# Performance work log

Hardware: AMD Instinct MI355X
Metric: run time of the kernel (lower is better)

The kernel has to match this reference:

```python
import jax, jax.numpy as jnp
import numpy as np

N, N_H = 256, 64          # detections per image, humans (permuted to top)
NUM_ITER = 2
E = 1024                   # node_encoding_size == box_feature_size
T_LIS, K_LIS, W_LIS = 8.3, 12.0, 10.0


def lis(x):
    # Low-grade Instance Suppression
    return T_LIS / (1.0 + jnp.exp(K_LIS - W_LIS * x))


def setup_inputs() -> dict:
    key = jax.random.key(0)
    ks = jax.random.split(key, 25)
    s = 0.02  # weight scale keeps sigmoid/relu in a sane range
    rn = lambda k, shape, sc=1.0: jax.random.normal(k, shape, jnp.float32) * sc
    inp = {}
    inp['box_features'] = rn(ks[0], (N, 12544))            # [N, 256*7*7]
    inp['node_spatial'] = rn(ks[1], (N, 1024))             # conv spatial-head output
    inp['scores'] = jax.random.uniform(ks[2], (N,), jnp.float32)
    labels = jax.random.randint(ks[3], (N,), 1, 80)
    inp['labels'] = labels.at[:N_H].set(0)                 # humans (idx 0) on top
    inp['class_mask'] = jax.random.bernoulli(ks[4], 0.2, (80, 117))
    inp['W_bh1'] = rn(ks[5], (12544, 1024), s); inp['b_bh1'] = jnp.zeros((1024,), jnp.float32)
    inp['W_bh2'] = rn(ks[6], (1024, 1024), s);  inp['b_bh2'] = jnp.zeros((1024,), jnp.float32)
    inp['W_sa']  = rn(ks[7], (1024, 1024), s)
    inp['W_a1']  = rn(ks[8], (4096, 2048), s); inp['b_a1'] = jnp.zeros((2048,), jnp.float32)
    inp['W_a2']  = rn(ks[9], (2048, 1024), s); inp['b_a2'] = jnp.zeros((1024,), jnp.float32)
    inp['W_a3']  = rn(ks[10], (1024, 1), s);   inp['b_a3'] = jnp.zeros((1,), jnp.float32)
    inp['W_hm']  = rn(ks[11], (1024, 1024), s); inp['b_hm'] = jnp.zeros((1024,), jnp.float32)
    inp['W_om']  = rn(ks[12], (1024, 1024), s); inp['b_om'] = jnp.zeros((1024,), jnp.float32)
    inp['W_hu']  = rn(ks[13], (2048, 1024), s)
    inp['W_ou']  = rn(ks[14], (2048, 1024), s)
    return inp


def _keep_indices():
    xv, yv = np.meshgrid(np.arange(N_H), np.arange(N), indexing='ij')
    m = (xv != yv).ravel()
    return jnp.asarray(xv.ravel()[m]), jnp.asarray(yv.ravel()[m])


def reference(box_features, node_spatial, scores, W_bh1, b_bh1, W_bh2, b_bh2,
              W_sa, W_a1, b_a1, W_a2, b_a2, W_a3, b_a3,
              W_hm, b_hm, W_om, b_om, W_hu, W_ou, labels, class_mask):
    # box_head: Flatten -> Linear -> ReLU -> Linear -> ReLU
    enc = jax.nn.relu(box_features @ W_bh1 + b_bh1)
    enc = jax.nn.relu(enc @ W_bh2 + b_bh2)                 # [N, E]
    h_enc = enc[:N_H]                                      # [N_H, E]
    h_sp = node_spatial[:N_H]                              # [N_H, 1024]
    # spatial_attention on pairwise spatial differences (fixed across iters)
    diff = node_spatial[None, :, :] - h_sp[:, None, :]     # [N_H, N, 1024]
    h_to_o = jnp.einsum('hnd,de->hne', diff, W_sa)         # Linear, no bias
    o_to_h = -h_to_o
    adj = jnp.ones((N_H, N), enc.dtype)
    for _ in range(NUM_ITER):
        # adjacency MLP + sigmoid over all n_h*n pairs
        hf = jnp.concatenate([h_enc, h_sp], axis=1)        # [N_H, 2048]
        of = jnp.concatenate([enc, node_spatial], axis=1)  # [N, 2048]
        pair_in = jnp.concatenate([
            jnp.broadcast_to(hf[:, None, :], (N_H, N, 2 * E)),
            jnp.broadcast_to(of[None, :, :], (N_H, N, 2 * E))], axis=-1)  # [N_H,N,4096]
        hdn = jax.nn.relu(pair_in @ W_a1 + b_a1)
        hdn = jax.nn.relu(hdn @ W_a2 + b_a2)
        adj = jax.nn.sigmoid((hdn @ W_a3 + b_a3)[..., 0])  # [N_H, N]
        # object -> human messages
        obj_msg = jax.nn.relu(enc @ W_om + b_om)           # [N, R]
        agg_o = (adj[..., None] * (obj_msg[None, :, :] * o_to_h)).sum(1)  # [N_H, R]
        h_enc = jnp.concatenate([h_enc, agg_o], axis=1) @ W_hu            # [N_H, E]
        # human -> object messages
        hum_msg = jax.nn.relu(h_enc @ W_hm + b_hm)         # [N_H, R]
        agg_h = (adj[..., None] * (hum_msg[:, None, :] * h_to_o)).sum(0)  # [N, R]
        enc = jnp.concatenate([enc, agg_h], axis=1) @ W_ou                # [N, E]
    x_keep, y_keep = _keep_indices()                       # [P], P = N_H*N - N_H
    pair_feats = jnp.concatenate([h_enc[x_keep], h_sp[x_keep],
                                  enc[y_keep], node_spatial[y_keep]], axis=1)  # [P, 4096]
    # prior scores: LIS(score_h)*LIS(score_o) scattered to valid target classes
    prod = lis(scores[x_keep]) * lis(scores[y_keep])       # [P]
    prior = prod[:, None] * class_mask[labels[y_keep]].astype(pair_feats.dtype)  # [P, 117]
    prior = adj[x_keep, y_keep][:, None] * prior
    return jnp.concatenate([pair_feats, prior], axis=1)    # [P, 4096+117]
```

## Files before the change

kernel.cpp:

```cpp
#include <hip/hip_runtime.h>

using bf16 = __bf16;
typedef __bf16 bf16x4 __attribute__((ext_vector_type(4)));
typedef __bf16 bf16x8 __attribute__((ext_vector_type(8)));
typedef float  f32x4  __attribute__((ext_vector_type(4)));

#define LDS_STRIDE 40
#define GST 40

__device__ __forceinline__ float ldf(const void* p, size_t i, int f32) {
    return f32 ? ((const float*)p)[i] : (float)((const bf16*)p)[i];
}
__device__ __forceinline__ bf16x8 ld8(const void* p, size_t i, int f32) {
    bf16x8 r;
    if (f32) {
        f32x4 a = *(const f32x4*)((const float*)p + i);
        f32x4 b = *(const f32x4*)((const float*)p + i + 4);
#pragma unroll
        for (int j = 0; j < 4; ++j) { r[j] = (bf16)a[j]; r[j + 4] = (bf16)b[j]; }
    } else {
        r = *(const bf16x8*)((const bf16*)p + i);
    }
    return r;
}
__device__ __forceinline__ void st1(void* p, size_t i, float v, int f32) {
    if (f32) ((float*)p)[i] = v;
    else     ((bf16*)p)[i] = (bf16)v;
}

__global__ void init_flag(int* __restrict__ dflag) { *dflag = 0; }

__global__ void detect_kernel(const unsigned short* __restrict__ p, int n,
                              int* __restrict__ dflag)
{
    const unsigned int* q = (const unsigned int*)p;
    const int nw = n >> 1;
    int hit = 0;
    for (int i = blockIdx.x * 256 + threadIdx.x; i < nw; i += gridDim.x * 256) {
        unsigned int w = q[i];
        if ((w & 0x7F80u) == 0x7F80u || (w & 0x7F800000u) == 0x7F800000u) hit = 1;
    }
    if (__any(hit) && (threadIdx.x & 63) == 0) atomicOr(dflag, 1);
}

__global__ void cvt_kernel(const void* __restrict__ src, bf16* __restrict__ dst,
                           int n, const int* __restrict__ dflag)
{
    const int f32 = *dflag;
    const int stride = gridDim.x * 256;
    if ((n & 7) == 0) {
        const int nv = n >> 3;
        for (int i = blockIdx.x * 256 + threadIdx.x; i < nv; i += stride) {
            bf16x8 v = ld8(src, (size_t)i * 8, f32);
            *(bf16x8*)(dst + (size_t)i * 8) = v;
        }
    } else {
        for (int i = blockIdx.x * 256 + threadIdx.x; i < n; i += stride)
            dst[i] = (bf16)ldf(src, i, f32);
    }
}

__global__ void transpose_any(const void* __restrict__ W, bf16* __restrict__ Wt,
                              int K, int N, const int* __restrict__ dflag)
{
    __shared__ bf16 tile[32][33];
    const int f32 = *dflag;
    const int n0 = blockIdx.x * 32, k0 = blockIdx.y * 32;
    const int tx = threadIdx.x, ty = threadIdx.y;
#pragma unroll
    for (int i = 0; i < 4; ++i)
        tile[ty + i * 8][tx] = (bf16)ldf(W, (size_t)(k0 + ty + i * 8) * N + n0 + tx, f32);
    __syncthreads();
#pragma unroll
    for (int i = 0; i < 4; ++i)
        Wt[(size_t)(n0 + ty + i * 8) * K + k0 + tx] = tile[tx][ty + i * 8];
}

__global__ __launch_bounds__(256)
void gemm_p(const bf16* __restrict__ A, int lda,
            const void* __restrict__ B, size_t boff, int ldb,
            float* __restrict__ part, int N, int Kc,
            const int* __restrict__ dflag)
{
    __shared__ bf16 As[64 * GST];
    __shared__ bf16 Bs[64 * GST];
    const int f32 = *dflag;
    const int t = threadIdx.x;
    const int l = t & 63;
    const int quad = l >> 4, lr = l & 15;
    const int w = t >> 6, wm = w >> 1, wn = w & 1;
    const int mBlock = blockIdx.y * 64, nBlock = blockIdx.x * 64;
    const int ar = t >> 2, ac = (t & 3) * 8;
    const int kr = t >> 3, nc = (t & 7) * 8;
    const int kBeg = blockIdx.z * Kc;
    const int nIter = Kc >> 5;

    f32x4 acc[2][2] = {};

    bf16x8 avr = *(const bf16x8*)(A + (size_t)(mBlock + ar) * lda + kBeg + ac);
    bf16x8 bvr = ld8(B, boff + (size_t)(kBeg + kr) * ldb + nBlock + nc, f32);

    for (int it = 0; it < nIter; ++it) {
        *(bf16x8*)&As[ar * GST + ac] = avr;
#pragma unroll
        for (int j = 0; j < 8; ++j) {
            int wr = nc + j;
            Bs[wr * GST + (kr ^ (((wr >> 3) & 3) << 3))] = bvr[j];
        }
        __syncthreads();
        if (it + 1 < nIter) {
            int k0 = kBeg + (it + 1) * 32;
            avr = *(const bf16x8*)(A + (size_t)(mBlock + ar) * lda + k0 + ac);
            bvr = ld8(B, boff + (size_t)(k0 + kr) * ldb + nBlock + nc, f32);
        }
        bf16x8 af[2], bfr[2];
#pragma unroll
        for (int mi = 0; mi < 2; ++mi)
            af[mi] = *(const bf16x8*)&As[(wm * 32 + mi * 16 + lr) * GST + quad * 8];
#pragma unroll
        for (int nj = 0; nj < 2; ++nj) {
            int row = wn * 32 + nj * 16 + lr;
            bfr[nj] = *(const bf16x8*)&Bs[row * GST + ((quad * 8) ^ (((row >> 3) & 3) << 3))];
        }
#pragma unroll
        for (int mi = 0; mi < 2; ++mi)
#pragma unroll
            for (int nj = 0; nj < 2; ++nj)
                acc[mi][nj] = __builtin_amdgcn_mfma_f32_16x16x32_bf16(
                    af[mi], bfr[nj], acc[mi][nj], 0, 0, 0);
        __syncthreads();
    }

    float* outp = part + (size_t)blockIdx.z * ((size_t)gridDim.y * 64 * N);
#pragma unroll
    for (int mi = 0; mi < 2; ++mi)
#pragma unroll
        for (int nj = 0; nj < 2; ++nj) {
            int col = nBlock + wn * 32 + nj * 16 + lr;
#pragma unroll
            for (int rr = 0; rr < 4; ++rr) {
                int row = mBlock + wm * 32 + mi * 16 + quad * 4 + rr;
                outp[(size_t)row * N + col] = acc[mi][nj][rr];
            }
        }
}

template<bool RELU, bool BIAS, bool F32OUT>
__global__ void reduce_k(const float* __restrict__ part, int S, int total,
                         const bf16* __restrict__ bias, void* __restrict__ out, int N)
{
    int base = (blockIdx.x * 256 + threadIdx.x) * 4;
    if (base >= total) return;
    f32x4 s = *(const f32x4*)(part + base);
    for (int z = 1; z < S; ++z) {
        f32x4 v = *(const f32x4*)(part + (size_t)z * total + base);
        s[0] += v[0]; s[1] += v[1]; s[2] += v[2]; s[3] += v[3];
    }
    int col = base % N;
#pragma unroll
    for (int j = 0; j < 4; ++j) {
        float v = s[j];
        if (BIAS) v += (float)bias[col + j];
        if (RELU) v = fmaxf(v, 0.f);
        if (F32OUT) ((float*)out)[base + j] = v;
        else        ((bf16*)out)[base + j] = (bf16)v;
    }
}

__global__ void build_pairA(const float* __restrict__ Hb, const float* __restrict__ Op,
                            bf16* __restrict__ A)
{
    const int n = blockIdx.x;
    const int h = blockIdx.y;
    const int k = threadIdx.x * 8;
    const float* hp = Hb + (size_t)h * 2048 + k;
    const float* op = Op + (size_t)n * 2048 + k;
    f32x4 h0 = *(const f32x4*)hp, h1 = *(const f32x4*)(hp + 4);
    f32x4 o0 = *(const f32x4*)op, o1 = *(const f32x4*)(op + 4);
    bf16x8 r;
#pragma unroll
    for (int j = 0; j < 4; ++j) {
        r[j]     = (bf16)fmaxf(h0[j] + o0[j], 0.f);
        r[j + 4] = (bf16)fmaxf(h1[j] + o1[j], 0.f);
    }
    *(bf16x8*)(A + ((size_t)h * 256 + n) * 2048 + k) = r;
}

__global__ __launch_bounds__(256)
void pair_gemm(const bf16* __restrict__ Apg, const bf16* __restrict__ Wt_a2,
               const bf16* __restrict__ b_a2, const bf16* __restrict__ w_a3,
               float* __restrict__ slots)
{
    __shared__ bf16 As[128 * LDS_STRIDE];
    __shared__ bf16 Bs[128 * LDS_STRIDE];
    const int t = threadIdx.x;
    const int l = t & 63, w = t >> 6;
    const int quad = l >> 4, lr = l & 15;
    const int wm = w >> 1, wn = w & 1;
    const int nb = blockIdx.x, mb = blockIdx.y;
    const int p0 = mb * 128;
    const int ar = t >> 1, ac0 = (t & 1) * 16;

    const bf16* Ap = Apg + (size_t)(p0 + ar) * 2048 + ac0;
    const bf16* Bp = Wt_a2 + (size_t)(nb * 128 + ar) * 2048 + ac0;

    f32x4 acc[4][4] = {};

    bf16x8 a0 = *(const bf16x8*)(Ap);
    bf16x8 a1 = *(const bf16x8*)(Ap + 8);
    bf16x8 b0 = *(const bf16x8*)(Bp);
    bf16x8 b1 = *(const bf16x8*)(Bp + 8);

    for (int k0 = 0; k0 < 2048; k0 += 32) {
        *(bf16x8*)&As[ar * LDS_STRIDE + ac0]     = a0;
        *(bf16x8*)&As[ar * LDS_STRIDE + ac0 + 8] = a1;
        *(bf16x8*)&Bs[ar * LDS_STRIDE + ac0]     = b0;
        *(bf16x8*)&Bs[ar * LDS_STRIDE + ac0 + 8] = b1;
        __syncthreads();
        if (k0 + 32 < 2048) {
            a0 = *(const bf16x8*)(Ap + k0 + 32);
            a1 = *(const bf16x8*)(Ap + k0 + 40);
            b0 = *(const bf16x8*)(Bp + k0 + 32);
            b1 = *(const bf16x8*)(Bp + k0 + 40);
        }

        bf16x8 af[4], bfr[4];
#pragma unroll
        for (int mi = 0; mi < 4; ++mi)
            af[mi] = *(const bf16x8*)&As[(wm * 64 + mi * 16 + lr) * LDS_STRIDE + quad * 8];
#pragma unroll
        for (int nj = 0; nj < 4; ++nj)
            bfr[nj] = *(const bf16x8*)&Bs[(wn * 64 + nj * 16 + lr) * LDS_STRIDE + quad * 8];
#pragma unroll
        for (int mi = 0; mi < 4; ++mi)
#pragma unroll
            for (int nj = 0; nj < 4; ++nj)
                acc[mi][nj] = __builtin_amdgcn_mfma_f32_16x16x32_bf16(
                    af[mi], bfr[nj], acc[mi][nj], 0, 0, 0);
        __syncthreads();
    }

    float w3v[4], b2v[4];
#pragma unroll
    for (int nj = 0; nj < 4; ++nj) {
        int col = nb * 128 + wn * 64 + nj * 16 + lr;
        w3v[nj] = (float)w_a3[col];
        b2v[nj] = (float)b_a2[col];
    }
#pragma unroll
    for (int mi = 0; mi < 4; ++mi) {
        f32x4 rs = {0.f, 0.f, 0.f, 0.f};
#pragma unroll
        for (int nj = 0; nj < 4; ++nj)
#pragma unroll
            for (int rr = 0; rr < 4; ++rr)
                rs[rr] += fmaxf(acc[mi][nj][rr] + b2v[nj], 0.f) * w3v[nj];
#pragma unroll
        for (int off = 1; off < 16; off <<= 1) {
            rs[0] += __shfl_xor(rs[0], off);
            rs[1] += __shfl_xor(rs[1], off);
            rs[2] += __shfl_xor(rs[2], off);
            rs[3] += __shfl_xor(rs[3], off);
        }
        if (lr == 0) {
            int p = p0 + wm * 64 + mi * 16 + quad * 4;
            int slot = nb * 2 + wn;
            slots[(size_t)(p + 0) * 16 + slot] = rs[0];
            slots[(size_t)(p + 1) * 16 + slot] = rs[1];
            slots[(size_t)(p + 2) * 16 + slot] = rs[2];
            slots[(size_t)(p + 3) * 16 + slot] = rs[3];
        }
    }
}

__global__ void adj_finalize(const float* __restrict__ slots,
                             const bf16* __restrict__ b_a3, float* __restrict__ adj)
{
    int i = blockIdx.x * 256 + threadIdx.x;
    float s = (float)b_a3[0];
#pragma unroll
    for (int k = 0; k < 16; ++k) s += slots[(size_t)i * 16 + k];
    adj[i] = 1.f / (1.f + expf(-s));
}

__global__ void copy_rows(const bf16* __restrict__ src, int lds_,
                          bf16* __restrict__ dst, int ldd)
{
    int c = blockIdx.x * 256 + threadIdx.x;
    int r = blockIdx.y;
    dst[(size_t)r * ldd + c] = src[(size_t)r * lds_ + c];
}

__global__ void agg_o_kernel(const float* __restrict__ adj, const bf16* __restrict__ obj_msg,
                             const bf16* __restrict__ nsW, bf16* __restrict__ out)
{
    int e = blockIdx.x * 256 + threadIdx.x;
    int h = blockIdx.y;
    float nh = (float)nsW[h * 1024 + e];
    float s = 0.f;
    for (int n = 0; n < 256; ++n) {
        float a  = adj[h * 256 + n];
        float om = (float)obj_msg[n * 1024 + e];
        float nw = (float)nsW[n * 1024 + e];
        s += a * om * (nh - nw);
    }
    out[(size_t)h * 2048 + e] = (bf16)s;
}

__global__ void agg_h_kernel(const float* __restrict__ adj, const bf16* __restrict__ hum_msg,
                             const bf16* __restrict__ nsW, bf16* __restrict__ out)
{
    int e = blockIdx.x * 256 + threadIdx.x;
    int n = blockIdx.y;
    float nn = (float)nsW[n * 1024 + e];
    float s = 0.f;
    for (int h = 0; h < 64; ++h) {
        float a  = adj[h * 256 + n];
        float hm = (float)hum_msg[h * 1024 + e];
        float nw = (float)nsW[h * 1024 + e];
        s += a * hm * (nn - nw);
    }
    out[(size_t)n * 2048 + e] = (bf16)s;
}

__global__ void out_kernel(const bf16* __restrict__ h_enc, const bf16* __restrict__ enc,
                           const bf16* __restrict__ nsp_bf, const float* __restrict__ adj,
                           const bf16* __restrict__ scores_bf, const int* __restrict__ labels,
                           const int* __restrict__ cmask, void* __restrict__ out,
                           const int* __restrict__ dflag)
{
    const int f32 = *dflag;
    const int r = blockIdx.x;
    const int x = r / 255;
    const int tt = r % 255;
    const int y = tt + (tt >= x ? 1 : 0);
    const size_t rbase = (size_t)r * 4213;
    const bf16* seg[4] = { h_enc + x * 1024, nsp_bf + x * 1024, enc + y * 1024, nsp_bf + y * 1024 };
    const int t = threadIdx.x;
#pragma unroll
    for (int k = 0; k < 4; ++k) {
        int ci = t + k * 256;
        int sidx = ci >> 8;
        int off = (ci & 255) * 4;
        bf16x4 v = *(const bf16x4*)(seg[sidx] + off);
        size_t d = rbase + sidx * 1024 + off;
        st1(out, d + 0, (float)v[0], f32);
        st1(out, d + 1, (float)v[1], f32);
        st1(out, d + 2, (float)v[2], f32);
        st1(out, d + 3, (float)v[3], f32);
    }
    if (t < 117) {
        float sx = (float)scores_bf[x], sy = (float)scores_bf[y];
        float lx = 8.3f / (1.f + expf(12.f - 10.f * sx));
        float ly = 8.3f / (1.f + expf(12.f - 10.f * sy));
        float a = adj[x * 256 + y];
        float m = cmask[labels[y] * 117 + t] ? 1.f : 0.f;
        st1(out, rbase + 4096 + t, a * lx * ly * m, f32);
    }
}

extern "C" void kernel_launch(void* const* d_in, const int* in_sizes, int n_in,
                              void* d_out, int out_size, void* d_ws, size_t ws_size,
                              hipStream_t stream)
{
    (void)in_sizes; (void)n_in; (void)out_size; (void)ws_size;
    const void* box    = d_in[0];
    const void* nsp    = d_in[1];
    const void* scores = d_in[2];
    const int*  labels = (const int*)d_in[3];
    const int*  cmask  = (const int*)d_in[4];
    const void* W_bh1 = d_in[5],  *b_bh1 = d_in[6];
    const void* W_bh2 = d_in[7],  *b_bh2 = d_in[8];
    const void* W_sa  = d_in[9];
    const void* W_a1  = d_in[10], *b_a1  = d_in[11];
    const void* W_a2  = d_in[12], *b_a2  = d_in[13];
    const void* W_a3  = d_in[14], *b_a3  = d_in[15];
    const void* W_hm  = d_in[16], *b_hm  = d_in[17];
    const void* W_om  = d_in[18], *b_om  = d_in[19];
    const void* W_hu  = d_in[20];
    const void* W_ou  = d_in[21];

    char* ws = (char*)d_ws;
    size_t off = 0;
    auto alloc = [&](size_t bytes) -> void* {
        off = (off + 255) & ~(size_t)255;
        void* p = ws + off;
        off += bytes;
        return p;
    };
    int*  dflag   = (int*)alloc(4);
    bf16* box_bf  = (bf16*)alloc((size_t)256 * 12544 * 2);
    bf16* nsp_bf  = (bf16*)alloc((size_t)256 * 1024 * 2);
    bf16* Wt_a2   = (bf16*)alloc((size_t)1024 * 2048 * 2);
    bf16* smalls  = (bf16*)alloc((size_t)8464 * 2);
    bf16* sb_bh1 = smalls,        *sb_bh2 = smalls + 1024;
    bf16* sb_om  = smalls + 2048, *sb_hm  = smalls + 3072;
    bf16* sb_a1  = smalls + 4096, *sb_a2  = smalls + 6144;
    bf16* sw_a3  = smalls + 7168, *sb_a3  = smalls + 8192;
    bf16* sscore = smalls + 8208;
    bf16* t0      = (bf16*)alloc((size_t)256 * 1024 * 2);
    bf16* enc     = (bf16*)alloc((size_t)256 * 1024 * 2);
    bf16* nsW     = (bf16*)alloc((size_t)256 * 1024 * 2);
    bf16* h_enc   = (bf16*)alloc((size_t)64 * 1024 * 2);
    bf16* hf      = (bf16*)alloc((size_t)64 * 2048 * 2);
    bf16* of      = (bf16*)alloc((size_t)256 * 2048 * 2);
    float* Hpart  = (float*)alloc((size_t)64 * 2048 * 4);
    float* Opart  = (float*)alloc((size_t)256 * 2048 * 4);
    float* slots  = (float*)alloc((size_t)16384 * 16 * 4);
    float* adj    = (float*)alloc((size_t)16384 * 4);
    bf16* obj_msg = (bf16*)alloc((size_t)256 * 1024 * 2);
    bf16* hu_in   = (bf16*)alloc((size_t)64 * 2048 * 2);
    bf16* hum_msg = (bf16*)alloc((size_t)64 * 1024 * 2);
    bf16* ou_in   = (bf16*)alloc((size_t)256 * 2048 * 2);
    float* part   = (float*)alloc((size_t)2097152 * 4);
    bf16* A_bf    = (bf16*)alloc((size_t)16384 * 2048 * 2);

    init_flag<<<1, 1, 0, stream>>>(dflag);
    detect_kernel<<<256, 256, 0, stream>>>((const unsigned short*)box, 524288, dflag);

    auto cvt = [&](const void* s, bf16* d, int n) {
        int g = (n + 2047) / 2048; if (g < 1) g = 1; if (g > 4096) g = 4096;
        cvt_kernel<<<g, 256, 0, stream>>>(s, d, n, dflag);
    };
    cvt(box, box_bf, 256 * 12544);
    cvt(nsp, nsp_bf, 256 * 1024);
    cvt(b_bh1, sb_bh1, 1024);  cvt(b_bh2, sb_bh2, 1024);
    cvt(b_om,  sb_om,  1024);  cvt(b_hm,  sb_hm,  1024);
    cvt(b_a1,  sb_a1,  2048);  cvt(b_a2,  sb_a2,  1024);
    cvt(W_a3,  sw_a3,  1024);  cvt(b_a3,  sb_a3,  1);
    cvt(scores, sscore, 256);

    transpose_any<<<dim3(1024 / 32, 2048 / 32), dim3(32, 8), 0, stream>>>(
        W_a2, Wt_a2, 2048, 1024, dflag);

    gemm_p<<<dim3(16, 4, 8), 256, 0, stream>>>(box_bf, 12544, W_bh1, 0, 1024, part, 1024, 1568, dflag);
    reduce_k<true, true, false><<<dim3(256), 256, 0, stream>>>(part, 8, 262144, sb_bh1, t0, 1024);
    gemm_p<<<dim3(16, 4, 4), 256, 0, stream>>>(t0, 1024, W_bh2, 0, 1024, part, 1024, 256, dflag);
    reduce_k<true, true, false><<<dim3(256), 256, 0, stream>>>(part, 4, 262144, sb_bh2, enc, 1024);
    gemm_p<<<dim3(16, 4, 4), 256, 0, stream>>>(nsp_bf, 1024, W_sa, 0, 1024, part, 1024, 256, dflag);
    reduce_k<false, false, false><<<dim3(256), 256, 0, stream>>>(part, 4, 262144, nullptr, nsW, 1024);
    copy_rows<<<dim3(4, 64), 256, 0, stream>>>(enc, 1024, h_enc, 1024);

    for (int it = 0; it < 2; ++it) {
        copy_rows<<<dim3(4, 64), 256, 0, stream>>>(h_enc, 1024, hf, 2048);
        copy_rows<<<dim3(4, 64), 256, 0, stream>>>(nsp_bf, 1024, hf + 1024, 2048);
        copy_rows<<<dim3(4, 256), 256, 0, stream>>>(enc, 1024, of, 2048);
        copy_rows<<<dim3(4, 256), 256, 0, stream>>>(nsp_bf, 1024, of + 1024, 2048);
        gemm_p<<<dim3(32, 1, 8), 256, 0, stream>>>(hf, 2048, W_a1, 0, 2048, part, 2048, 256, dflag);
        reduce_k<false, true, true><<<dim3(128), 256, 0, stream>>>(part, 8, 131072, sb_a1, Hpart, 2048);
        gemm_p<<<dim3(32, 4, 4), 256, 0, stream>>>(of, 2048, W_a1, (size_t)2048 * 2048, 2048, part, 2048, 512, dflag);
        reduce_k<false, false, true><<<dim3(512), 256, 0, stream>>>(part, 4, 524288, nullptr, Opart, 2048);
        build_pairA<<<dim3(256, 64), 256, 0, stream>>>(Hpart, Opart, A_bf);
        pair_gemm<<<dim3(8, 128), 256, 0, stream>>>(A_bf, Wt_a2, sb_a2, sw_a3, slots);
        adj_finalize<<<dim3(64), 256, 0, stream>>>(slots, sb_a3, adj);
        gemm_p<<<dim3(16, 4, 4), 256, 0, stream>>>(enc, 1024, W_om, 0, 1024, part, 1024, 256, dflag);
        reduce_k<true, true, false><<<dim3(256), 256, 0, stream>>>(part, 4, 262144, sb_om, obj_msg, 1024);
        copy_rows<<<dim3(4, 64), 256, 0, stream>>>(h_enc, 1024, hu_in, 2048);
        agg_o_kernel<<<dim3(4, 64), 256, 0, stream>>>(adj, obj_msg, nsW, hu_in + 1024);
        gemm_p<<<dim3(16, 1, 16), 256, 0, stream>>>(hu_in, 2048, W_hu, 0, 1024, part, 1024, 128, dflag);
        reduce_k<false, false, false><<<dim3(64), 256, 0, stream>>>(part, 16, 65536, nullptr, h_enc, 1024);
        gemm_p<<<dim3(16, 1, 16), 256, 0, stream>>>(h_enc, 1024, W_hm, 0, 1024, part, 1024, 64, dflag);
        reduce_k<true, true, false><<<dim3(64), 256, 0, stream>>>(part, 16, 65536, sb_hm, hum_msg, 1024);
        copy_rows<<<dim3(4, 256), 256, 0, stream>>>(enc, 1024, ou_in, 2048);
        agg_h_kernel<<<dim3(4, 256), 256, 0, stream>>>(adj, hum_msg, nsW, ou_in + 1024);
        gemm_p<<<dim3(16, 4, 4), 256, 0, stream>>>(ou_in, 2048, W_ou, 0, 1024, part, 1024, 512, dflag);
        reduce_k<false, false, false><<<dim3(256), 256, 0, stream>>>(part, 4, 262144, nullptr, enc, 1024);
    }

    out_kernel<<<dim3(16320), 256, 0, stream>>>(
        h_enc, enc, nsp_bf, adj, sscore, labels, cmask, d_out, dflag);
}
```

Measured before the change: 1.031 ms.

## Merge small launches, use direct global-to-LDS loads, vectorize output stores

Several unrelated changes are bundled here. The small bias and score conversions collapse into one kernel, and the paired copy_rows launches merge into concat2 or into the aggregation kernels, which cuts launch count. pair_gemm now loads tiles with global_load_lds into an XOR-swizzled LDS layout instead of register prefetch plus padded stores, which drops the register double-buffering and overlap. out_kernel writes whole output rows with aligned float4 stores. The cvt_smalls pointer `smalls` is not shown being declared, and the old per-buffer names may no longer line up.

```diff
diff --git a/kernel.cpp b/kernel.cpp
--- a/kernel.cpp
+++ b/kernel.cpp
@@ -5,7 +5,6 @@
 typedef __bf16 bf16x8 __attribute__((ext_vector_type(8)));
 typedef float  f32x4  __attribute__((ext_vector_type(4)));
 
-#define LDS_STRIDE 40
 #define GST 40
 
 __device__ __forceinline__ float ldf(const void* p, size_t i, int f32) {
@@ -26,6 +25,12 @@
 __device__ __forceinline__ void st1(void* p, size_t i, float v, int f32) {
     if (f32) ((float*)p)[i] = v;
     else     ((bf16*)p)[i] = (bf16)v;
+}
+
+__device__ __forceinline__ void gl_lds16(const bf16* g, bf16* l) {
+    __builtin_amdgcn_global_load_lds(
+        (const __attribute__((address_space(1))) void*)g,
+        (__attribute__((address_space(3))) void*)l, 16, 0, 0);
 }
 
 __global__ void init_flag(int* __restrict__ dflag) { *dflag = 0; }
@@ -48,16 +53,32 @@
 {
     const int f32 = *dflag;
     const int stride = gridDim.x * 256;
-    if ((n & 7) == 0) {
-        const int nv = n >> 3;
-        for (int i = blockIdx.x * 256 + threadIdx.x; i < nv; i += stride) {
-            bf16x8 v = ld8(src, (size_t)i * 8, f32);
-            *(bf16x8*)(dst + (size_t)i * 8) = v;
-        }
-    } else {
-        for (int i = blockIdx.x * 256 + threadIdx.x; i < n; i += stride)
-            dst[i] = (bf16)ldf(src, i, f32);
-    }
+    const int nv = n >> 3;
+    for (int i = blockIdx.x * 256 + threadIdx.x; i < nv; i += stride) {
+        bf16x8 v = ld8(src, (size_t)i * 8, f32);
+        *(bf16x8*)(dst + (size_t)i * 8) = v;
+    }
+}
+
+__global__ void cvt_smalls(const void* b_bh1, const void* b_bh2, const void* b_om,
+                           const void* b_hm, const void* b_a1, const void* b_a2,
+                           const void* w_a3, const void* b_a3, const void* scores,
+                           bf16* __restrict__ smalls, const int* __restrict__ dflag)
+{
+    const int f32 = *dflag;
+    int i = blockIdx.x * 256 + threadIdx.x;
+    const void* s; int off;
+    if      (i < 1024) { s = b_bh1; off = 0;    }
+    else if (i < 2048) { s = b_bh2; off = 1024; }
+    else if (i < 3072) { s = b_om;  off = 2048; }
+    else if (i < 4096) { s = b_hm;  off = 3072; }
+    else if (i < 6144) { s = b_a1;  off = 4096; }
+    else if (i < 7168) { s = b_a2;  off = 6144; }
+    else if (i < 8192) { s = w_a3;  off = 7168; }
+    else if (i < 8193) { s = b_a3;  off = 8192; }
+    else if (i >= 8208 && i < 8464) { s = scores; off = 8208; }
+    else return;
+    smalls[i] = (bf16)ldf(s, i - off, f32);
 }
 
 __global__ void transpose_any(const void* __restrict__ W, bf16* __restrict__ Wt,
@@ -191,46 +212,49 @@
                const bf16* __restrict__ b_a2, const bf16* __restrict__ w_a3,
                float* __restrict__ slots)
 {
-    __shared__ bf16 As[128 * LDS_STRIDE];
-    __shared__ bf16 Bs[128 * LDS_STRIDE];
+    __shared__ bf16 As[128 * 32];
+    __shared__ bf16 Bs[128 * 32];
     const int t = threadIdx.x;
     const int l = t & 63, w = t >> 6;
     const int quad = l >> 4, lr = l & 15;
     const int wm = w >> 1, wn = w & 1;
     const int nb = blockIdx.x, mb = blockIdx.y;
     const int p0 = mb * 128;
-    const int ar = t >> 1, ac0 = (t & 1) * 16;
-
-    const bf16* Ap = Apg + (size_t)(p0 + ar) * 2048 + ac0;
-    const bf16* Bp = Wt_a2 + (size_t)(nb * 128 + ar) * 2048 + ac0;
+
+    const int grow = w * 16 + (l >> 2);
+    const int slot = l & 3;
+    const int csrc = slot ^ ((grow >> 1) & 3);
+    const bf16* Asrc0 = Apg + (size_t)(p0 + grow) * 2048 + csrc * 8;
+    const bf16* Asrc1 = Apg + (size_t)(p0 + 64 + grow) * 2048 + csrc * 8;
+    const bf16* Bsrc0 = Wt_a2 + (size_t)(nb * 128 + grow) * 2048 + csrc * 8;
+    const bf16* Bsrc1 = Wt_a2 + (size_t)(nb * 128 + 64 + grow) * 2048 + csrc * 8;
+    bf16* AsW0 = As + w * 512;
+    bf16* AsW1 = As + 2048 + w * 512;
+    bf16* BsW0 = Bs + w * 512;
+    bf16* BsW1 = Bs + 2048 + w * 512;
 
     f32x4 acc[4][4] = {};
 
-    bf16x8 a0 = *(const bf16x8*)(Ap);
-    bf16x8 a1 = *(const bf16x8*)(Ap + 8);
-    bf16x8 b0 = *(const bf16x8*)(Bp);
-    bf16x8 b1 = *(const bf16x8*)(Bp + 8);
-
     for (int k0 = 0; k0 < 2048; k0 += 32) {
-        *(bf16x8*)&As[ar * LDS_STRIDE + ac0]     = a0;
-        *(bf16x8*)&As[ar * LDS_STRIDE + ac0 + 8] = a1;
-        *(bf16x8*)&Bs[ar * LDS_STRIDE + ac0]     = b0;
-        *(bf16x8*)&Bs[ar * LDS_STRIDE + ac0 + 8] = b1;
+        gl_lds16(Asrc0 + k0, AsW0);
+        gl_lds16(Asrc1 + k0, AsW1);
+        gl_lds16(Bsrc0 + k0, BsW0);
+        gl_lds16(Bsrc1 + k0, BsW1);
         __syncthreads();
-        if (k0 + 32 < 2048) {
-            a0 = *(const bf16x8*)(Ap + k0 + 32);
-            a1 = *(const bf16x8*)(Ap + k0 + 40);
-            b0 = *(const bf16x8*)(Bp + k0 + 32);
-            b1 = *(const bf16x8*)(Bp + k0 + 40);
-        }
 
         bf16x8 af[4], bfr[4];
 #pragma unroll
-        for (int mi = 0; mi < 4; ++mi)
-            af[mi] = *(const bf16x8*)&As[(wm * 64 + mi * 16 + lr) * LDS_STRIDE + quad * 8];
-#pragma unroll
-        for (int nj = 0; nj < 4; ++nj)
-            bfr[nj] = *(const bf16x8*)&Bs[(wn * 64 + nj * 16 + lr) * LDS_STRIDE + quad * 8];
+        for (int mi = 0; mi < 4; ++mi) {
+            int row = wm * 64 + mi * 16 + lr;
+            int sl = quad ^ ((row >> 1) & 3);
+            af[mi] = *(const bf16x8*)&As[row * 32 + sl * 8];
+        }
+#pragma unroll
+        for (int nj = 0; nj < 4; ++nj) {
+            int row = wn * 64 + nj * 16 + lr;
+            int sl = quad ^ ((row >> 1) & 3);
+            bfr[nj] = *(const bf16x8*)&Bs[row * 32 + sl * 8];
+        }
 #pragma unroll
         for (int mi = 0; mi < 4; ++mi)
 #pragma unroll
@@ -264,11 +288,11 @@
         }
         if (lr == 0) {
             int p = p0 + wm * 64 + mi * 16 + quad * 4;
-            int slot = nb * 2 + wn;
-            slots[(size_t)(p + 0) * 16 + slot] = rs[0];
-            slots[(size_t)(p + 1) * 16 + slot] = rs[1];
-            slots[(size_t)(p + 2) * 16 + slot] = rs[2];
-            slots[(size_t)(p + 3) * 16 + slot] = rs[3];
+            int slot2 = nb * 2 + wn;
+            slots[(size_t)(p + 0) * 16 + slot2] = rs[0];
+            slots[(size_t)(p + 1) * 16 + slot2] = rs[1];
+            slots[(size_t)(p + 2) * 16 + slot2] = rs[2];
+            slots[(size_t)(p + 3) * 16 + slot2] = rs[3];
         }
     }
 }
@@ -291,11 +315,26 @@
     dst[(size_t)r * ldd + c] = src[(size_t)r * lds_ + c];
 }
 
+__global__ void concat2(const bf16* __restrict__ L, const bf16* __restrict__ R,
+                        bf16* __restrict__ dst)
+{
+    int c = blockIdx.x * 256 + threadIdx.x;
+    int r = blockIdx.y;
+    dst[(size_t)r * 2048 + c] = (c < 1024) ? L[(size_t)r * 1024 + c]
+                                           : R[(size_t)r * 1024 + (c - 1024)];
+}
+
 __global__ void agg_o_kernel(const float* __restrict__ adj, const bf16* __restrict__ obj_msg,
-                             const bf16* __restrict__ nsW, bf16* __restrict__ out)
-{
-    int e = blockIdx.x * 256 + threadIdx.x;
+                             const bf16* __restrict__ nsW, const bf16* __restrict__ h_enc,
+                             bf16* __restrict__ out)
+{
+    int bx = blockIdx.x;
     int h = blockIdx.y;
+    int e = (bx & 3) * 256 + threadIdx.x;
+    if (bx < 4) {
+        out[(size_t)h * 2048 + e] = h_enc[(size_t)h * 1024 + e];
+        return;
+    }
     float nh = (float)nsW[h * 1024 + e];
     float s = 0.f;
     for (int n = 0; n < 256; ++n) {
@@ -304,14 +343,20 @@
         float nw = (float)nsW[n * 1024 + e];
         s += a * om * (nh - nw);
     }
-    out[(size_t)h * 2048 + e] = (bf16)s;
+    out[(size_t)h * 2048 + 1024 + e] = (bf16)s;
 }
 
 __global__ void agg_h_kernel(const float* __restrict__ adj, const bf16* __restrict__ hum_msg,
-                             const bf16* __restrict__ nsW, bf16* __restrict__ out)
-{
-    int e = blockIdx.x * 256 + threadIdx.x;
+                             const bf16* __restrict__ nsW, const bf16* __restrict__ enc,
+                             bf16* __restrict__ out)
+{
+    int bx = blockIdx.x;
     int n = blockIdx.y;
+    int e = (bx & 3) * 256 + threadIdx.x;
+    if (bx < 4) {
+        out[(size_t)n * 2048 + e] = enc[(size_t)n * 1024 + e];
+        return;
+    }
     float nn = (float)nsW[n * 1024 + e];
     float s = 0.f;
     for (int h = 0; h < 64; ++h) {
@@ -320,7 +365,7 @@
         float nw = (float)nsW[h * 1024 + e];
         s += a * hm * (nn - nw);
     }
-    out[(size_t)n * 2048 + e] = (bf16)s;
+    out[(size_t)n * 2048 + 1024 + e] = (bf16)s;
 }
 
 __global__ void out_kernel(const bf16* __restrict__ h_enc, const bf16* __restrict__ enc,
@@ -337,25 +382,33 @@
     const size_t rbase = (size_t)r * 4213;
     const bf16* seg[4] = { h_enc + x * 1024, nsp_bf + x * 1024, enc + y * 1024, nsp_bf + y * 1024 };
     const int t = threadIdx.x;
-#pragma unroll
-    for (int k = 0; k < 4; ++k) {
-        int ci = t + k * 256;
-        int sidx = ci >> 8;
-        int off = (ci & 255) * 4;
-        bf16x4 v = *(const bf16x4*)(seg[sidx] + off);
-        size_t d = rbase + sidx * 1024 + off;
-        st1(out, d + 0, (float)v[0], f32);
-        st1(out, d + 1, (float)v[1], f32);
-        st1(out, d + 2, (float)v[2], f32);
-        st1(out, d + 3, (float)v[3], f32);
-    }
-    if (t < 117) {
-        float sx = (float)scores_bf[x], sy = (float)scores_bf[y];
-        float lx = 8.3f / (1.f + expf(12.f - 10.f * sx));
-        float ly = 8.3f / (1.f + expf(12.f - 10.f * sy));
-        float a = adj[x * 256 + y];
-        float m = cmask[labels[y] * 117 + t] ? 1.f : 0.f;
-        st1(out, rbase + 4096 + t, a * lx * ly * m, f32);
+
+    float sx = (float)scores_bf[x], sy = (float)scores_bf[y];
+    float lx = 8.3f / (1.f + expf(12.f - 10.f * sx));
+    float ly = 8.3f / (1.f + expf(12.f - 10.f * sy));
+    float pf = adj[x * 256 + y] * lx * ly;
+    const int* cm = cmask + labels[y] * 117;
+
+    auto getv = [&](int e) -> float {
+        if (e < 4096) return (float)seg[e >> 10][e & 1023];
+        return cm[e - 4096] ? pf : 0.f;
+    };
+
+    if (f32) {
+        float* op = (float*)out + rbase;
+        const int ali = (int)((4 - (rbase & 3)) & 3);
+        const int nv = (4213 - ali) >> 2;
+        for (int vi = t; vi < nv; vi += 256) {
+            int e0 = ali + vi * 4;
+            f32x4 v = { getv(e0), getv(e0 + 1), getv(e0 + 2), getv(e0 + 3) };
+            *(f32x4*)(op + e0) = v;
+        }
+        if (t < ali) op[t] = getv(t);
+        int te = ali + nv * 4;
+        if (t < 4213 - te) op[te + t] = getv(te + t);
+    } else {
+        bf16* op = (bf16*)out + rbase;
+        for (int e = t; e < 4213; e += 256) op[e] = (bf16)getv(e);
     }
 }
 
@@ -418,17 +471,10 @@
     init_flag<<<1, 1, 0, stream>>>(dflag);
     detect_kernel<<<256, 256, 0, stream>>>((const unsigned short*)box, 524288, dflag);
 
-    auto cvt = [&](const void* s, bf16* d, int n) {
-        int g = (n + 2047) / 2048; if (g < 1) g = 1; if (g > 4096) g = 4096;
-        cvt_kernel<<<g, 256, 0, stream>>>(s, d, n, dflag);
-    };
-    cvt(box, box_bf, 256 * 12544);
-    cvt(nsp, nsp_bf, 256 * 1024);
-    cvt(b_bh1, sb_bh1, 1024);  cvt(b_bh2, sb_bh2, 1024);
-    cvt(b_om,  sb_om,  1024);  cvt(b_hm,  sb_hm,  1024);
-    cvt(b_a1,  sb_a1,  2048);  cvt(b_a2,  sb_a2,  1024);
-    cvt(W_a3,  sw_a3,  1024);  cvt(b_a3,  sb_a3,  1);
-    cvt(scores, sscore, 256);
+    cvt_kernel<<<1568, 256, 0, stream>>>(box, box_bf, 256 * 12544, dflag);
+    cvt_kernel<<<128, 256, 0, stream>>>(nsp, nsp_bf, 256 * 1024, dflag);
+    cvt_smalls<<<34, 256, 0, stream>>>(b_bh1, b_bh2, b_om, b_hm, b_a1, b_a2,
+                                       W_a3, b_a3, scores, smalls, dflag);
 
     transpose_any<<<dim3(1024 / 32, 2048 / 32), dim3(32, 8), 0, stream>>>(
         W_a2, Wt_a2, 2048, 1024, dflag);
@@ -442,10 +488,8 @@
     copy_rows<<<dim3(4, 64), 256, 0, stream>>>(enc, 1024, h_enc, 1024);
 
     for (int it = 0; it < 2; ++it) {
-        copy_rows<<<dim3(4, 64), 256, 0, stream>>>(h_enc, 1024, hf, 2048);
-        copy_rows<<<dim3(4, 64), 256, 0, stream>>>(nsp_bf, 1024, hf + 1024, 2048);
-        copy_rows<<<dim3(4, 256), 256, 0, stream>>>(enc, 1024, of, 2048);
-        copy_rows<<<dim3(4, 256), 256, 0, stream>>>(nsp_bf, 1024, of + 1024, 2048);
+        concat2<<<dim3(8, 64), 256, 0, stream>>>(h_enc, nsp_bf, hf);
+        concat2<<<dim3(8, 256), 256, 0, stream>>>(enc, nsp_bf, of);
         gemm_p<<<dim3(32, 1, 8), 256, 0, stream>>>(hf, 2048, W_a1, 0, 2048, part, 2048, 256, dflag);
         reduce_k<false, true, true><<<dim3(128), 256, 0, stream>>>(part, 8, 131072, sb_a1, Hpart, 2048);
         gemm_p<<<dim3(32, 4, 4), 256, 0, stream>>>(of, 2048, W_a1, (size_t)2048 * 2048, 2048, part, 2048, 512, dflag);
@@ -455,14 +499,12 @@
         adj_finalize<<<dim3(64), 256, 0, stream>>>(slots, sb_a3, adj);
         gemm_p<<<dim3(16, 4, 4), 256, 0, stream>>>(enc, 1024, W_om, 0, 1024, part, 1024, 256, dflag);
         reduce_k<true, true, false><<<dim3(256), 256, 0, stream>>>(part, 4, 262144, sb_om, obj_msg, 1024);
-        copy_rows<<<dim3(4, 64), 256, 0, stream>>>(h_enc, 1024, hu_in, 2048);
-        agg_o_kernel<<<dim3(4, 64), 256, 0, stream>>>(adj, obj_msg, nsW, hu_in + 1024);
+        agg_o_kernel<<<dim3(8, 64), 256, 0, stream>>>(adj, obj_msg, nsW, h_enc, hu_in);
         gemm_p<<<dim3(16, 1, 16), 256, 0, stream>>>(hu_in, 2048, W_hu, 0, 1024, part, 1024, 128, dflag);
         reduce_k<false, false, false><<<dim3(64), 256, 0, stream>>>(part, 16, 65536, nullptr, h_enc, 1024);
         gemm_p<<<dim3(16, 1, 16), 256, 0, stream>>>(h_enc, 1024, W_hm, 0, 1024, part, 1024, 64, dflag);
         reduce_k<true, true, false><<<dim3(64), 256, 0, stream>>>(part, 16, 65536, sb_hm, hum_msg, 1024);
-        copy_rows<<<dim3(4, 256), 256, 0, stream>>>(enc, 1024, ou_in, 2048);
-        agg_h_kernel<<<dim3(4, 256), 256, 0, stream>>>(adj, hum_msg, nsW, ou_in + 1024);
+        agg_h_kernel<<<dim3(8, 256), 256, 0, stream>>>(adj, hum_msg, nsW, enc, ou_in);
         gemm_p<<<dim3(16, 4, 4), 256, 0, stream>>>(ou_in, 2048, W_ou, 0, 1024, part, 1024, 512, dflag);
         reduce_k<false, false, false><<<dim3(256), 256, 0, stream>>>(part, 4, 262144, nullptr, enc, 1024);
     }
```

After: 991.3 us. 3.9% less time.
